# Kernel optimization log

Hardware: AMD Instinct MI355X
Metric: run time of the kernel (lower is better)

The kernel has to match this reference:

```python
import jax, jax.numpy as jnp
import numpy as np


def setup_inputs() -> dict:
    key = jax.random.key(0)
    k1, k2, k3 = jax.random.split(key, 3)
    B, T, S, D = 16, 1024, 1024, 1024
    inp = jax.random.normal(k1, (B, T, D), dtype=jnp.float32)
    ctx = jax.random.normal(k2, (B, S, D), dtype=jnp.float32)
    # nn.Linear(dim, dim, bias=False) weight, applied as x @ W.T
    W_in = jax.random.normal(k3, (D, D), dtype=jnp.float32) * (1.0 / np.sqrt(D))
    return {"input": inp, "context": ctx, "W_in": W_in}


def reference(input, context, W_in):
    # h_t = linear_in(input): [B,T,D] @ W_in.T
    h_t = jnp.einsum("btd,ed->bte", input, W_in)
    # align scores: [B,T,S]
    align = jnp.einsum("btd,bsd->bts", h_t, context)
    align_vectors = jax.nn.softmax(align, axis=-1)
    # context-weighted sum: [B,T,D]
    attn_h = jnp.einsum("bts,bsd->btd", align_vectors, context)
    # non-one-step path: transpose(0,1)
    attn_h = jnp.transpose(attn_h, (1, 0, 2))          # [T,B,D]
    align_vectors = jnp.transpose(align_vectors, (1, 0, 2))  # [T,B,S]
    return attn_h, align_vectors
```

## Files before the change

### kernel.cpp

```cpp
#include <hip/hip_runtime.h>
#include <hip/hip_bf16.h>

using short8 = __attribute__((ext_vector_type(8))) short;
using half8  = __attribute__((ext_vector_type(8))) _Float16;
using f32x4  = __attribute__((ext_vector_type(4))) float;

constexpr int Bdim = 16;
constexpr int Tdim = 1024;
constexpr int Sdim = 1024;
constexpr int Ddim = 1024;

__device__ __forceinline__ unsigned short f2hu(float x) {
  _Float16 h = (_Float16)x;
  return __builtin_bit_cast(unsigned short, h);
}
__device__ __forceinline__ float hu2f(unsigned short u) {
  return (float)__builtin_bit_cast(_Float16, u);
}

__global__ void __launch_bounds__(256)
conv_kernel(const float* __restrict__ src, unsigned short* __restrict__ dst, int n4) {
  int i = blockIdx.x * blockDim.x + threadIdx.x;
  int stride = gridDim.x * blockDim.x;
  for (; i < n4; i += stride) {
    float4 v = reinterpret_cast<const float4*>(src)[i];
    ushort4 h;
    h.x = f2hu(v.x); h.y = f2hu(v.y); h.z = f2hu(v.z); h.w = f2hu(v.w);
    reinterpret_cast<ushort4*>(dst)[i] = h;
  }
}

__global__ void __launch_bounds__(256)
ctxprep_kernel(const float* __restrict__ ctx, unsigned short* __restrict__ ctx16,
               unsigned short* __restrict__ ctxT) {
  __shared__ float tile[64][65];
  int b = blockIdx.z;
  int d0 = blockIdx.x * 64, s0 = blockIdx.y * 64;
  const float* src = ctx + (size_t)b * Sdim * Ddim;
  unsigned short* dstS = ctx16 + (size_t)b * Sdim * Ddim;
  unsigned short* dstT = ctxT + (size_t)b * Ddim * Sdim;
  int tx = threadIdx.x & 15, ty = threadIdx.x >> 4;
  #pragma unroll
  for (int r = 0; r < 4; ++r) {
    int s = ty + r * 16;
    float4 v = reinterpret_cast<const float4*>(src + (size_t)(s0 + s) * Ddim + d0)[tx];
    ushort4 hs;
    hs.x = f2hu(v.x); hs.y = f2hu(v.y); hs.z = f2hu(v.z); hs.w = f2hu(v.w);
    reinterpret_cast<ushort4*>(dstS + (size_t)(s0 + s) * Ddim + d0)[tx] = hs;
    tile[s][tx * 4 + 0] = v.x; tile[s][tx * 4 + 1] = v.y;
    tile[s][tx * 4 + 2] = v.z; tile[s][tx * 4 + 3] = v.w;
  }
  __syncthreads();
  #pragma unroll
  for (int r = 0; r < 4; ++r) {
    int d = ty + r * 16;
    ushort4 o;
    o.x = f2hu(tile[tx * 4 + 0][d]);
    o.y = f2hu(tile[tx * 4 + 1][d]);
    o.z = f2hu(tile[tx * 4 + 2][d]);
    o.w = f2hu(tile[tx * 4 + 3][d]);
    reinterpret_cast<ushort4*>(dstT + (size_t)(d0 + d) * Sdim + s0)[tx] = o;
  }
}

#define MFMAH(d, x, y)                                                          \
  d = __builtin_amdgcn_mfma_f32_16x16x32_f16(__builtin_bit_cast(half8, (x)),    \
                                             __builtin_bit_cast(half8, (y)), (d), 0, 0, 0)

#define GLOADLDS(g, l)                                                          \
  __builtin_amdgcn_global_load_lds((const __attribute__((address_space(1))) void*)(g), \
                                   (__attribute__((address_space(3))) void*)(l), 16, 0, 0)

template <int MODE>
__global__ void __launch_bounds__(512, 2)
gemmP(const unsigned short* __restrict__ Ag, const unsigned short* __restrict__ Bg,
      size_t aBatch, size_t bBatch, int mnShift,
      unsigned short* __restrict__ outHi, unsigned short* __restrict__ outLo,
      float* __restrict__ outF) {
  constexpr int NT = 16;
  __shared__ __align__(16) unsigned short lds[2 * 2 * 16384];

  const int hw = blockIdx.x;
  const int L  = (hw & 7) * 32 + (hw >> 3);
  const int bb = L >> mnShift;
  const int r  = L & ((1 << mnShift) - 1);
  const int m0 = (r >> 2) * 256;
  const int n0 = (r & 3) * 256;

  const int tid  = threadIdx.x;
  const int lane = tid & 63;
  const int w    = tid >> 6;
  const int wr   = (w >> 2) * 128;
  const int wc   = (w & 3) * 64;
  const int l15  = lane & 15;
  const int g0   = lane >> 4;
  const int r7   = l15 & 7;

  const int srow8 = tid >> 3;
  const int sg    = tid & 7;
  const int rs    = srow8 & 7;
  const unsigned short* spA = Ag + (size_t)bb * aBatch + (size_t)(m0 + srow8) * 1024 + ((sg ^ rs) * 8);
  const unsigned short* spB = Bg + (size_t)bb * bBatch + (size_t)(n0 + srow8) * 1024 + ((sg ^ rs) * 8);

  auto stage = [&](int buf, int kt) {
    #pragma unroll
    for (int i = 0; i < 4; ++i) {
      unsigned short* lb = lds + buf * 32768 + (srow8 + i * 64) * 64 + sg * 8;
      GLOADLDS(spA + (size_t)i * (64 * 1024) + kt * 64, lb);
      GLOADLDS(spB + (size_t)i * (64 * 1024) + kt * 64, lb + 16384);
    }
  };

  f32x4 acc[8][4];
  const f32x4 vzero = {0.f, 0.f, 0.f, 0.f};
  #pragma unroll
  for (int f = 0; f < 8; ++f)
    #pragma unroll
    for (int j = 0; j < 4; ++j) acc[f][j] = vzero;

  stage(0, 0);

  #pragma unroll 1
  for (int t = 0; t < NT; ++t) {
    stage((t + 1) & 1, (t + 1 < NT) ? (t + 1) : (NT - 1));
    asm volatile("s_waitcnt vmcnt(8)" ::: "memory");
    __builtin_amdgcn_s_barrier();
    asm volatile("" ::: "memory");
    const unsigned short* tb = lds + (t & 1) * 32768;
    const unsigned short* tB = tb + 16384;

    short8 bf[4][2];
    #pragma unroll
    for (int j = 0; j < 4; ++j)
      #pragma unroll
      for (int kk = 0; kk < 2; ++kk) {
        const int row = wc + j * 16 + l15;
        bf[j][kk] = *reinterpret_cast<const short8*>(tB + row * 64 + ((kk * 4 + g0) ^ r7) * 8);
      }
    #pragma unroll
    for (int fp = 0; fp < 4; ++fp) {
      short8 af[2][2];
      #pragma unroll
      for (int f2 = 0; f2 < 2; ++f2) {
        const int row = wr + (fp * 2 + f2) * 16 + l15;
        #pragma unroll
        for (int kk = 0; kk < 2; ++kk)
          af[f2][kk] = *reinterpret_cast<const short8*>(tb + row * 64 + ((kk * 4 + g0) ^ r7) * 8);
      }
      __builtin_amdgcn_s_setprio(1);
      #pragma unroll
      for (int f2 = 0; f2 < 2; ++f2)
        #pragma unroll
        for (int j = 0; j < 4; ++j)
          #pragma unroll
          for (int kk = 0; kk < 2; ++kk)
            MFMAH(acc[fp * 2 + f2][j], af[f2][kk], bf[j][kk]);
      __builtin_amdgcn_s_setprio(0);
    }
    asm volatile("s_waitcnt lgkmcnt(0)" ::: "memory");
    __builtin_amdgcn_sched_barrier(0);
    __builtin_amdgcn_s_barrier();
  }

  const int lr = (lane >> 4) * 4;
  const int lc = lane & 15;
  #pragma unroll
  for (int f = 0; f < 8; ++f)
    #pragma unroll
    for (int j = 0; j < 4; ++j)
      #pragma unroll
      for (int q = 0; q < 4; ++q) {
        int rr = m0 + wr + f * 16 + lr + q;
        int cc = n0 + wc + j * 16 + lc;
        float v = acc[f][j][q];
        if constexpr (MODE == 0) {
          unsigned short h = f2hu(v);
          unsigned short l = f2hu(v - hu2f(h));
          outHi[(size_t)rr * 1024 + cc] = h;
          outLo[(size_t)rr * 1024 + cc] = l;
        } else {
          outF[((size_t)rr * 16 + bb) * 1024 + cc] = v;
        }
      }
}

__global__ void __launch_bounds__(512, 2)
gemmS(const unsigned short* __restrict__ Ah, const unsigned short* __restrict__ Al,
      const unsigned short* __restrict__ Bh,
      size_t aBatch, size_t bBatch, int mnShift,
      float* __restrict__ outF) {
  constexpr int NT = 16;
  __shared__ __align__(16) unsigned short lds[5 * 16384];

  const int hw = blockIdx.x;
  const int L  = (hw & 7) * 32 + (hw >> 3);
  const int bb = L >> mnShift;
  const int r  = L & ((1 << mnShift) - 1);
  const int m0 = (r >> 2) * 256;
  const int n0 = (r & 3) * 256;

  const int tid  = threadIdx.x;
  const int lane = tid & 63;
  const int w    = tid >> 6;
  const int wr   = (w >> 2) * 128;
  const int wc   = (w & 3) * 64;
  const int l15  = lane & 15;
  const int g0   = lane >> 4;
  const int r7   = l15 & 7;

  const int srow8 = tid >> 3;
  const int sg    = tid & 7;
  const int rs    = srow8 & 7;
  const size_t aRow = (size_t)bb * aBatch + (size_t)(m0 + srow8) * 1024 + ((sg ^ rs) * 8);
  const unsigned short* spAh = Ah + aRow;
  const unsigned short* spAl = Al + aRow;
  const unsigned short* spB  = Bh + (size_t)bb * bBatch + (size_t)(n0 + srow8) * 1024 + ((sg ^ rs) * 8);

  auto stageA = [&](int buf, int kt) {
    #pragma unroll
    for (int i = 0; i < 4; ++i) {
      unsigned short* lb = lds + buf * 32768 + (srow8 + i * 64) * 64 + sg * 8;
      GLOADLDS(spAh + (size_t)i * (64 * 1024) + kt * 64, lb);
      GLOADLDS(spAl + (size_t)i * (64 * 1024) + kt * 64, lb + 16384);
    }
  };
  auto stageB = [&](int kt) {
    #pragma unroll
    for (int i = 0; i < 4; ++i) {
      unsigned short* lb = lds + 65536 + (srow8 + i * 64) * 64 + sg * 8;
      GLOADLDS(spB + (size_t)i * (64 * 1024) + kt * 64, lb);
    }
  };

  f32x4 acc[8][4];
  const f32x4 vzero = {0.f, 0.f, 0.f, 0.f};
  #pragma unroll
  for (int f = 0; f < 8; ++f)
    #pragma unroll
    for (int j = 0; j < 4; ++j) acc[f][j] = vzero;

  stageA(0, 0);
  stageB(0);

  #pragma unroll 1
  for (int t = 0; t < NT; ++t) {
    const int tn = (t + 1 < NT) ? t + 1 : NT - 1;
    stageA((t + 1) & 1, tn);
    asm volatile("s_waitcnt vmcnt(8)" ::: "memory");
    __builtin_amdgcn_s_barrier();
    asm volatile("" ::: "memory");
    const unsigned short* tA  = lds + (t & 1) * 32768;
    const unsigned short* tAl = tA + 16384;
    const unsigned short* tB  = lds + 65536;

    short8 bf[4][2];
    #pragma unroll
    for (int j = 0; j < 4; ++j)
      #pragma unroll
      for (int kk = 0; kk < 2; ++kk) {
        const int row = wc + j * 16 + l15;
        bf[j][kk] = *reinterpret_cast<const short8*>(tB + row * 64 + ((kk * 4 + g0) ^ r7) * 8);
      }
    short8 ah0[2][2], al0[2][2];
    #pragma unroll
    for (int f2 = 0; f2 < 2; ++f2) {
      const int row = wr + f2 * 16 + l15;
      #pragma unroll
      for (int kk = 0; kk < 2; ++kk) {
        const int po = ((kk * 4 + g0) ^ r7) * 8;
        ah0[f2][kk] = *reinterpret_cast<const short8*>(tA  + row * 64 + po);
        al0[f2][kk] = *reinterpret_cast<const short8*>(tAl + row * 64 + po);
      }
    }
    asm volatile("s_waitcnt lgkmcnt(0)" ::: "memory");
    __builtin_amdgcn_sched_barrier(0);
    __builtin_amdgcn_s_barrier();
    stageB(tn);
    __builtin_amdgcn_s_setprio(1);
    #pragma unroll
    for (int f2 = 0; f2 < 2; ++f2)
      #pragma unroll
      for (int j = 0; j < 4; ++j)
        #pragma unroll
        for (int kk = 0; kk < 2; ++kk) {
          MFMAH(acc[f2][j], ah0[f2][kk], bf[j][kk]);
          MFMAH(acc[f2][j], al0[f2][kk], bf[j][kk]);
        }
    __builtin_amdgcn_s_setprio(0);

    #pragma unroll
    for (int fp = 1; fp < 4; ++fp) {
      short8 ah[2][2], al[2][2];
      #pragma unroll
      for (int f2 = 0; f2 < 2; ++f2) {
        const int row = wr + (fp * 2 + f2) * 16 + l15;
        #pragma unroll
        for (int kk = 0; kk < 2; ++kk) {
          const int po = ((kk * 4 + g0) ^ r7) * 8;
          ah[f2][kk] = *reinterpret_cast<const short8*>(tA  + row * 64 + po);
          al[f2][kk] = *reinterpret_cast<const short8*>(tAl + row * 64 + po);
        }
      }
      __builtin_amdgcn_s_setprio(1);
      #pragma unroll
      for (int f2 = 0; f2 < 2; ++f2)
        #pragma unroll
        for (int j = 0; j < 4; ++j)
          #pragma unroll
          for (int kk = 0; kk < 2; ++kk) {
            MFMAH(acc[fp * 2 + f2][j], ah[f2][kk], bf[j][kk]);
            MFMAH(acc[fp * 2 + f2][j], al[f2][kk], bf[j][kk]);
          }
      __builtin_amdgcn_s_setprio(0);
    }
    asm volatile("s_waitcnt lgkmcnt(0)" ::: "memory");
    __builtin_amdgcn_sched_barrier(0);
    __builtin_amdgcn_s_barrier();
  }

  const int lr = (lane >> 4) * 4;
  const int lc = lane & 15;
  #pragma unroll
  for (int f = 0; f < 8; ++f)
    #pragma unroll
    for (int j = 0; j < 4; ++j)
      #pragma unroll
      for (int q = 0; q < 4; ++q) {
        int rr = m0 + wr + f * 16 + lr + q;
        int cc = n0 + wc + j * 16 + lc;
        outF[((size_t)rr * 16 + bb) * 1024 + cc] = acc[f][j][q];
      }
}

__global__ void __launch_bounds__(256)
softmax_kernel(float* __restrict__ av, unsigned short* __restrict__ p) {
  int row = blockIdx.x;
  int t = row >> 4, b = row & 15;
  float* a = av + (size_t)row * 1024;
  int tid = threadIdx.x, lane = tid & 63, wid = tid >> 6;
  float4 v = reinterpret_cast<float4*>(a)[tid];
  float mx = fmaxf(fmaxf(v.x, v.y), fmaxf(v.z, v.w));
  #pragma unroll
  for (int o = 1; o < 64; o <<= 1) mx = fmaxf(mx, __shfl_xor(mx, o));
  __shared__ float redM[4], redS[4];
  if (lane == 0) redM[wid] = mx;
  __syncthreads();
  mx = fmaxf(fmaxf(redM[0], redM[1]), fmaxf(redM[2], redM[3]));
  float e0 = __expf(v.x - mx), e1 = __expf(v.y - mx);
  float e2 = __expf(v.z - mx), e3 = __expf(v.w - mx);
  float s = (e0 + e1) + (e2 + e3);
  #pragma unroll
  for (int o = 1; o < 64; o <<= 1) s += __shfl_xor(s, o);
  if (lane == 0) redS[wid] = s;
  __syncthreads();
  s = (redS[0] + redS[1]) + (redS[2] + redS[3]);
  float inv = 1.0f / s;
  float4 o4;
  o4.x = e0 * inv; o4.y = e1 * inv; o4.z = e2 * inv; o4.w = e3 * inv;
  reinterpret_cast<float4*>(a)[tid] = o4;
  ushort4 pb;
  pb.x = f2hu(o4.x); pb.y = f2hu(o4.y); pb.z = f2hu(o4.z); pb.w = f2hu(o4.w);
  reinterpret_cast<ushort4*>(p + ((size_t)b * Tdim + t) * Sdim)[tid] = pb;
}

extern "C" void kernel_launch(void* const* d_in, const int* in_sizes, int n_in,
                              void* d_out, int out_size, void* d_ws, size_t ws_size,
                              hipStream_t stream) {
  const float* input = (const float*)d_in[0];
  const float* ctx   = (const float*)d_in[1];
  const float* Wt    = (const float*)d_in[2];
  float* attn_out  = (float*)d_out;
  float* align_out = attn_out + (size_t)Tdim * Bdim * Ddim;

  const size_t NE = (size_t)Bdim * Tdim * Ddim;
  unsigned short* x16 = (unsigned short*)d_ws;
  unsigned short* Wh  = x16 + NE;
  unsigned short* hh  = Wh + (size_t)Ddim * Ddim;
  unsigned short* hl  = hh + NE;
  unsigned short* ctxT = hl + NE;
  unsigned short* ctx16 = x16;
  unsigned short* p     = hh;

  conv_kernel<<<2048, 256, 0, stream>>>(input, x16, (int)(NE / 4));
  conv_kernel<<<512, 256, 0, stream>>>(Wt, Wh, (int)((size_t)Ddim * Ddim / 4));
  gemmP<0><<<256, 512, 0, stream>>>(x16, Wh, 0, 0, 8, hh, hl, nullptr);
  ctxprep_kernel<<<dim3(16, 16, Bdim), 256, 0, stream>>>(ctx, ctx16, ctxT);
  gemmS<<<256, 512, 0, stream>>>(hh, hl, ctx16, (size_t)Tdim * Ddim,
                                 (size_t)Sdim * Ddim, 4, align_out);
  softmax_kernel<<<Bdim * Tdim, 256, 0, stream>>>(align_out, p);
  gemmP<1><<<256, 512, 0, stream>>>(p, ctxT, (size_t)Tdim * Sdim,
                                    (size_t)Ddim * Sdim, 4, nullptr, nullptr, attn_out);
}
```

Baseline: 218.4 us.

## Fuse softmax into score GEMM and drop hi/lo split of projected query

Replaces the separate score GEMM and softmax kernels with one kernel. Each block computes a 64-row by full-1024-column score tile, then does the row max, exp, sum and normalize in registers with shuffle and LDS reductions, writing both the fp32 align output and the fp16 probabilities. It also stores the projected query h as a single fp16 array instead of a hi/lo pair, which halves the MFMAs and memory traffic of the score GEMM. The aim is to avoid writing and re-reading the fp32 score matrix. The trade-offs are lower accuracy in the logits and a much larger, single-buffered LDS tile for the context operand, which likely limits each CU to one block.

```diff
diff --git a/kernel.cpp b/kernel.cpp
--- a/kernel.cpp
+++ b/kernel.cpp
@@ -75,8 +75,7 @@
 __global__ void __launch_bounds__(512, 2)
 gemmP(const unsigned short* __restrict__ Ag, const unsigned short* __restrict__ Bg,
       size_t aBatch, size_t bBatch, int mnShift,
-      unsigned short* __restrict__ outHi, unsigned short* __restrict__ outLo,
-      float* __restrict__ outF) {
+      unsigned short* __restrict__ outH, float* __restrict__ outF) {
   constexpr int NT = 16;
   __shared__ __align__(16) unsigned short lds[2 * 2 * 16384];
 
@@ -173,11 +172,8 @@
         int rr = m0 + wr + f * 16 + lr + q;
         int cc = n0 + wc + j * 16 + lc;
         float v = acc[f][j][q];
-        if constexpr (MODE == 0) {
-          unsigned short h = f2hu(v);
-          unsigned short l = f2hu(v - hu2f(h));
-          outHi[(size_t)rr * 1024 + cc] = h;
-          outLo[(size_t)rr * 1024 + cc] = l;
+        if constexpr (MODE == 2) {
+          outH[(size_t)rr * 1024 + cc] = f2hu(v);
         } else {
           outF[((size_t)rr * 16 + bb) * 1024 + cc] = v;
         }
@@ -185,182 +181,176 @@
 }
 
 __global__ void __launch_bounds__(512, 2)
-gemmS(const unsigned short* __restrict__ Ah, const unsigned short* __restrict__ Al,
-      const unsigned short* __restrict__ Bh,
-      size_t aBatch, size_t bBatch, int mnShift,
-      float* __restrict__ outF) {
+gemmF(const unsigned short* __restrict__ Hh, const unsigned short* __restrict__ Cg,
+      float* __restrict__ alignOut, unsigned short* __restrict__ pOut) {
   constexpr int NT = 16;
-  __shared__ __align__(16) unsigned short lds[5 * 16384];
+  __shared__ __align__(16) unsigned short lds[2 * 4096 + 65536];
 
   const int hw = blockIdx.x;
   const int L  = (hw & 7) * 32 + (hw >> 3);
-  const int bb = L >> mnShift;
-  const int r  = L & ((1 << mnShift) - 1);
-  const int m0 = (r >> 2) * 256;
-  const int n0 = (r & 3) * 256;
+  const int bb = L >> 4;
+  const int m0 = (L & 15) * 64;
 
   const int tid  = threadIdx.x;
   const int lane = tid & 63;
   const int w    = tid >> 6;
-  const int wr   = (w >> 2) * 128;
-  const int wc   = (w & 3) * 64;
   const int l15  = lane & 15;
   const int g0   = lane >> 4;
-  const int r7   = l15 & 7;
-
-  const int srow8 = tid >> 3;
-  const int sg    = tid & 7;
-  const int rs    = srow8 & 7;
-  const size_t aRow = (size_t)bb * aBatch + (size_t)(m0 + srow8) * 1024 + ((sg ^ rs) * 8);
-  const unsigned short* spAh = Ah + aRow;
-  const unsigned short* spAl = Al + aRow;
-  const unsigned short* spB  = Bh + (size_t)bb * bBatch + (size_t)(n0 + srow8) * 1024 + ((sg ^ rs) * 8);
+
+  const int srow = tid >> 3;
+  const int sg   = tid & 7;
+  const int rs   = srow & 7;
+  const unsigned short* spA = Hh + (size_t)bb * (Tdim * Ddim) + (size_t)(m0 + srow) * 1024 + ((sg ^ rs) * 8);
+  const unsigned short* spB = Cg + (size_t)bb * (Sdim * Ddim) + (size_t)srow * 1024 + ((sg ^ rs) * 8);
+
+  unsigned short* const ldsB = lds + 8192;
 
   auto stageA = [&](int buf, int kt) {
-    #pragma unroll
-    for (int i = 0; i < 4; ++i) {
-      unsigned short* lb = lds + buf * 32768 + (srow8 + i * 64) * 64 + sg * 8;
-      GLOADLDS(spAh + (size_t)i * (64 * 1024) + kt * 64, lb);
-      GLOADLDS(spAl + (size_t)i * (64 * 1024) + kt * 64, lb + 16384);
-    }
+    GLOADLDS(spA + kt * 64, lds + buf * 4096 + tid * 8);
   };
   auto stageB = [&](int kt) {
     #pragma unroll
-    for (int i = 0; i < 4; ++i) {
-      unsigned short* lb = lds + 65536 + (srow8 + i * 64) * 64 + sg * 8;
-      GLOADLDS(spB + (size_t)i * (64 * 1024) + kt * 64, lb);
-    }
+    for (int i = 0; i < 16; ++i)
+      GLOADLDS(spB + (size_t)i * (64 * 1024) + kt * 64, ldsB + i * 4096 + tid * 8);
   };
 
-  f32x4 acc[8][4];
+  f32x4 acc[4][8];
   const f32x4 vzero = {0.f, 0.f, 0.f, 0.f};
   #pragma unroll
-  for (int f = 0; f < 8; ++f)
-    #pragma unroll
-    for (int j = 0; j < 4; ++j) acc[f][j] = vzero;
+  for (int f = 0; f < 4; ++f)
+    #pragma unroll
+    for (int j = 0; j < 8; ++j) acc[f][j] = vzero;
 
   stageA(0, 0);
   stageB(0);
+  stageA(1, 1);
+  asm volatile("s_waitcnt vmcnt(1)" ::: "memory");
+  __builtin_amdgcn_s_barrier();
 
   #pragma unroll 1
   for (int t = 0; t < NT; ++t) {
-    const int tn = (t + 1 < NT) ? t + 1 : NT - 1;
-    stageA((t + 1) & 1, tn);
-    asm volatile("s_waitcnt vmcnt(8)" ::: "memory");
-    __builtin_amdgcn_s_barrier();
-    asm volatile("" ::: "memory");
-    const unsigned short* tA  = lds + (t & 1) * 32768;
-    const unsigned short* tAl = tA + 16384;
-    const unsigned short* tB  = lds + 65536;
-
-    short8 bf[4][2];
-    #pragma unroll
-    for (int j = 0; j < 4; ++j)
-      #pragma unroll
-      for (int kk = 0; kk < 2; ++kk) {
-        const int row = wc + j * 16 + l15;
-        bf[j][kk] = *reinterpret_cast<const short8*>(tB + row * 64 + ((kk * 4 + g0) ^ r7) * 8);
-      }
-    short8 ah0[2][2], al0[2][2];
-    #pragma unroll
-    for (int f2 = 0; f2 < 2; ++f2) {
-      const int row = wr + f2 * 16 + l15;
-      #pragma unroll
-      for (int kk = 0; kk < 2; ++kk) {
-        const int po = ((kk * 4 + g0) ^ r7) * 8;
-        ah0[f2][kk] = *reinterpret_cast<const short8*>(tA  + row * 64 + po);
-        al0[f2][kk] = *reinterpret_cast<const short8*>(tAl + row * 64 + po);
-      }
+    const unsigned short* tA = lds + (t & 1) * 4096;
+
+    short8 bf[8][2];
+    #pragma unroll
+    for (int j = 0; j < 8; ++j) {
+      const int row = w * 128 + j * 16 + l15;
+      #pragma unroll
+      for (int kk = 0; kk < 2; ++kk)
+        bf[j][kk] = *reinterpret_cast<const short8*>(ldsB + row * 64 + ((kk * 4 + g0) ^ (row & 7)) * 8);
+    }
+    short8 af[4][2];
+    #pragma unroll
+    for (int f = 0; f < 4; ++f) {
+      const int row = f * 16 + l15;
+      #pragma unroll
+      for (int kk = 0; kk < 2; ++kk)
+        af[f][kk] = *reinterpret_cast<const short8*>(tA + row * 64 + ((kk * 4 + g0) ^ (row & 7)) * 8);
     }
     asm volatile("s_waitcnt lgkmcnt(0)" ::: "memory");
     __builtin_amdgcn_sched_barrier(0);
     __builtin_amdgcn_s_barrier();
-    stageB(tn);
+
+    if (t + 1 < NT) stageB(t + 1);
+    if (t + 2 < NT) stageA(t & 1, t + 2);
+
     __builtin_amdgcn_s_setprio(1);
     #pragma unroll
-    for (int f2 = 0; f2 < 2; ++f2)
-      #pragma unroll
-      for (int j = 0; j < 4; ++j)
+    for (int f = 0; f < 4; ++f)
+      #pragma unroll
+      for (int j = 0; j < 8; ++j)
         #pragma unroll
-        for (int kk = 0; kk < 2; ++kk) {
-          MFMAH(acc[f2][j], ah0[f2][kk], bf[j][kk]);
-          MFMAH(acc[f2][j], al0[f2][kk], bf[j][kk]);
-        }
+        for (int kk = 0; kk < 2; ++kk)
+          MFMAH(acc[f][j], af[f][kk], bf[j][kk]);
     __builtin_amdgcn_s_setprio(0);
 
-    #pragma unroll
-    for (int fp = 1; fp < 4; ++fp) {
-      short8 ah[2][2], al[2][2];
-      #pragma unroll
-      for (int f2 = 0; f2 < 2; ++f2) {
-        const int row = wr + (fp * 2 + f2) * 16 + l15;
-        #pragma unroll
-        for (int kk = 0; kk < 2; ++kk) {
-          const int po = ((kk * 4 + g0) ^ r7) * 8;
-          ah[f2][kk] = *reinterpret_cast<const short8*>(tA  + row * 64 + po);
-          al[f2][kk] = *reinterpret_cast<const short8*>(tAl + row * 64 + po);
-        }
-      }
-      __builtin_amdgcn_s_setprio(1);
-      #pragma unroll
-      for (int f2 = 0; f2 < 2; ++f2)
-        #pragma unroll
-        for (int j = 0; j < 4; ++j)
-          #pragma unroll
-          for (int kk = 0; kk < 2; ++kk) {
-            MFMAH(acc[fp * 2 + f2][j], ah[f2][kk], bf[j][kk]);
-            MFMAH(acc[fp * 2 + f2][j], al[f2][kk], bf[j][kk]);
-          }
-      __builtin_amdgcn_s_setprio(0);
-    }
-    asm volatile("s_waitcnt lgkmcnt(0)" ::: "memory");
-    __builtin_amdgcn_sched_barrier(0);
+    if (t + 1 < NT) {
+      if (t + 2 < NT) asm volatile("s_waitcnt vmcnt(1)" ::: "memory");
+      else            asm volatile("s_waitcnt vmcnt(0)" ::: "memory");
+    }
     __builtin_amdgcn_s_barrier();
   }
 
+  float* red = (float*)lds;
   const int lr = (lane >> 4) * 4;
-  const int lc = lane & 15;
-  #pragma unroll
-  for (int f = 0; f < 8; ++f)
-    #pragma unroll
-    for (int j = 0; j < 4; ++j)
-      #pragma unroll
-      for (int q = 0; q < 4; ++q) {
-        int rr = m0 + wr + f * 16 + lr + q;
-        int cc = n0 + wc + j * 16 + lc;
-        outF[((size_t)rr * 16 + bb) * 1024 + cc] = acc[f][j][q];
-      }
-}
-
-__global__ void __launch_bounds__(256)
-softmax_kernel(float* __restrict__ av, unsigned short* __restrict__ p) {
-  int row = blockIdx.x;
-  int t = row >> 4, b = row & 15;
-  float* a = av + (size_t)row * 1024;
-  int tid = threadIdx.x, lane = tid & 63, wid = tid >> 6;
-  float4 v = reinterpret_cast<float4*>(a)[tid];
-  float mx = fmaxf(fmaxf(v.x, v.y), fmaxf(v.z, v.w));
-  #pragma unroll
-  for (int o = 1; o < 64; o <<= 1) mx = fmaxf(mx, __shfl_xor(mx, o));
-  __shared__ float redM[4], redS[4];
-  if (lane == 0) redM[wid] = mx;
+
+  float rmax[4][4];
+  #pragma unroll
+  for (int f = 0; f < 4; ++f)
+    #pragma unroll
+    for (int q = 0; q < 4; ++q) {
+      float m = acc[f][0][q];
+      #pragma unroll
+      for (int j = 1; j < 8; ++j) m = fmaxf(m, acc[f][j][q]);
+      #pragma unroll
+      for (int o = 1; o < 16; o <<= 1) m = fmaxf(m, __shfl_xor(m, o));
+      rmax[f][q] = m;
+    }
+  if (l15 == 0) {
+    #pragma unroll
+    for (int f = 0; f < 4; ++f)
+      #pragma unroll
+      for (int q = 0; q < 4; ++q) red[(f * 16 + lr + q) * 8 + w] = rmax[f][q];
+  }
   __syncthreads();
-  mx = fmaxf(fmaxf(redM[0], redM[1]), fmaxf(redM[2], redM[3]));
-  float e0 = __expf(v.x - mx), e1 = __expf(v.y - mx);
-  float e2 = __expf(v.z - mx), e3 = __expf(v.w - mx);
-  float s = (e0 + e1) + (e2 + e3);
-  #pragma unroll
-  for (int o = 1; o < 64; o <<= 1) s += __shfl_xor(s, o);
-  if (lane == 0) redS[wid] = s;
+  #pragma unroll
+  for (int f = 0; f < 4; ++f)
+    #pragma unroll
+    for (int q = 0; q < 4; ++q) {
+      const float* rr = red + (f * 16 + lr + q) * 8;
+      float m = rr[0];
+      #pragma unroll
+      for (int k = 1; k < 8; ++k) m = fmaxf(m, rr[k]);
+      rmax[f][q] = m;
+    }
   __syncthreads();
-  s = (redS[0] + redS[1]) + (redS[2] + redS[3]);
-  float inv = 1.0f / s;
-  float4 o4;
-  o4.x = e0 * inv; o4.y = e1 * inv; o4.z = e2 * inv; o4.w = e3 * inv;
-  reinterpret_cast<float4*>(a)[tid] = o4;
-  ushort4 pb;
-  pb.x = f2hu(o4.x); pb.y = f2hu(o4.y); pb.z = f2hu(o4.z); pb.w = f2hu(o4.w);
-  reinterpret_cast<ushort4*>(p + ((size_t)b * Tdim + t) * Sdim)[tid] = pb;
+
+  float rsum[4][4];
+  #pragma unroll
+  for (int f = 0; f < 4; ++f)
+    #pragma unroll
+    for (int q = 0; q < 4; ++q) {
+      float s = 0.f;
+      #pragma unroll
+      for (int j = 0; j < 8; ++j) {
+        float e = __expf(acc[f][j][q] - rmax[f][q]);
+        acc[f][j][q] = e;
+        s += e;
+      }
+      #pragma unroll
+      for (int o = 1; o < 16; o <<= 1) s += __shfl_xor(s, o);
+      rsum[f][q] = s;
+    }
+  if (l15 == 0) {
+    #pragma unroll
+    for (int f = 0; f < 4; ++f)
+      #pragma unroll
+      for (int q = 0; q < 4; ++q) red[(f * 16 + lr + q) * 8 + w] = rsum[f][q];
+  }
+  __syncthreads();
+  #pragma unroll
+  for (int f = 0; f < 4; ++f)
+    #pragma unroll
+    for (int q = 0; q < 4; ++q) {
+      const float* rr = red + (f * 16 + lr + q) * 8;
+      float s = ((rr[0] + rr[1]) + (rr[2] + rr[3])) + ((rr[4] + rr[5]) + (rr[6] + rr[7]));
+      rsum[f][q] = 1.0f / s;
+    }
+
+  #pragma unroll
+  for (int f = 0; f < 4; ++f)
+    #pragma unroll
+    for (int q = 0; q < 4; ++q) {
+      const int row = m0 + f * 16 + lr + q;
+      float inv = rsum[f][q];
+      #pragma unroll
+      for (int j = 0; j < 8; ++j) {
+        const int cc = w * 128 + j * 16 + l15;
+        float v = acc[f][j][q] * inv;
+        alignOut[((size_t)row * 16 + bb) * 1024 + cc] = v;
+        pOut[((size_t)bb * 1024 + row) * 1024 + cc] = f2hu(v);
+      }
+    }
 }
 
 extern "C" void kernel_launch(void* const* d_in, const int* in_sizes, int n_in,
@@ -373,21 +363,18 @@
   float* align_out = attn_out + (size_t)Tdim * Bdim * Ddim;
 
   const size_t NE = (size_t)Bdim * Tdim * Ddim;
-  unsigned short* x16 = (unsigned short*)d_ws;
-  unsigned short* Wh  = x16 + NE;
-  unsigned short* hh  = Wh + (size_t)Ddim * Ddim;
-  unsigned short* hl  = hh + NE;
-  unsigned short* ctxT = hl + NE;
+  unsigned short* x16  = (unsigned short*)d_ws;
+  unsigned short* Wh   = x16 + NE;
+  unsigned short* hh   = Wh + (size_t)Ddim * Ddim;
+  unsigned short* ctxT = hh + NE;
   unsigned short* ctx16 = x16;
   unsigned short* p     = hh;
 
   conv_kernel<<<2048, 256, 0, stream>>>(input, x16, (int)(NE / 4));
   conv_kernel<<<512, 256, 0, stream>>>(Wt, Wh, (int)((size_t)Ddim * Ddim / 4));
-  gemmP<0><<<256, 512, 0, stream>>>(x16, Wh, 0, 0, 8, hh, hl, nullptr);
+  gemmP<2><<<256, 512, 0, stream>>>(x16, Wh, 0, 0, 8, hh, nullptr);
   ctxprep_kernel<<<dim3(16, 16, Bdim), 256, 0, stream>>>(ctx, ctx16, ctxT);
-  gemmS<<<256, 512, 0, stream>>>(hh, hl, ctx16, (size_t)Tdim * Ddim,
-                                 (size_t)Sdim * Ddim, 4, align_out);
-  softmax_kernel<<<Bdim * Tdim, 256, 0, stream>>>(align_out, p);
+  gemmF<<<256, 512, 0, stream>>>(hh, ctx16, align_out, p);
   gemmP<1><<<256, 512, 0, stream>>>(p, ctxT, (size_t)Tdim * Sdim,
-                                    (size_t)Ddim * Sdim, 4, nullptr, nullptr, attn_out);
-}
+                                    (size_t)Ddim * Sdim, 4, nullptr, attn_out);
+}
```

Measured after the change: 187.1 us. -14.3%, faster.
